# Performance work log

Hardware: AMD Instinct MI355X
Metric: run time of the kernel (lower is better)

Reference implementation:

```python
import jax, jax.numpy as jnp
import numpy as np

N, B, E, H = 16384, 16, 131072, 2
NPG = N // B  # nodes per graph
DIMS = [128, 256, 512]  # in==out channels per GAT layer


def setup_inputs() -> dict:
    key = jax.random.key(0)
    ks = iter(jax.random.split(key, 40))
    inp = {"node_feats": jax.random.normal(next(ks), (N, DIMS[0]), jnp.float32)}
    for l, d in enumerate(DIMS):
        s = 1.0 / np.sqrt(d)
        inp[f"W{l}"] = jax.random.normal(next(ks), (d, H * d), jnp.float32) * s
        inp[f"attnl{l}"] = jax.random.normal(next(ks), (H, d), jnp.float32) * 0.1
        inp[f"attnr{l}"] = jax.random.normal(next(ks), (H, d), jnp.float32) * 0.1
        inp[f"resW{l}"] = jax.random.normal(next(ks), (d, H * d), jnp.float32) * s
        inp[f"gamma{l}"] = jnp.ones((d,), jnp.float32)
        inp[f"beta{l}"] = jnp.zeros((d,), jnp.float32)
        inp[f"alpha{l}"] = jnp.ones((d,), jnp.float32)
    dst = jax.random.randint(next(ks), (E,), 0, N, jnp.int32)
    # source node sampled from the same graph as the destination
    src = (dst // NPG) * NPG + jax.random.randint(next(ks), (E,), 0, NPG, jnp.int32)
    inp["edge_src"] = src
    inp["edge_dst"] = dst
    inp["graph_ids"] = jnp.repeat(jnp.arange(B, dtype=jnp.int32), NPG)
    return inp


def _gat(x, W, al, ar, rW, src, dst, d):
    # x: [N, in]; W,rW: [in, H*d]; al,ar: [H,d]
    h = (x @ W).reshape(N, H, d)
    el = jnp.sum(h * al, -1)  # [N,H]
    er = jnp.sum(h * ar, -1)  # [N,H]
    e = jax.nn.leaky_relu(el[src] + er[dst], 0.2)  # [E,H]
    m = jax.ops.segment_max(e, dst, num_segments=N)
    ex = jnp.exp(e - m[dst])
    a = ex / jax.ops.segment_sum(ex, dst, num_segments=N)[dst]  # edge softmax
    out = jax.ops.segment_sum(h[src] * a[:, :, None], dst, num_segments=N)
    return out + (x @ rW).reshape(N, H, d)  # residual projection


def _gnorm(x, gamma, beta, alpha, eps=1e-5):
    # GraphNorm: (x - alpha*mean) / std * gamma + beta, stats over all nodes/heads
    mean = jnp.mean(x, axis=(0, 1), keepdims=True)
    sh = x - alpha * mean
    var = jnp.mean(sh * sh, axis=(0, 1), keepdims=True)
    return gamma * sh * jax.lax.rsqrt(var + eps) + beta


def reference(node_feats, W0, attnl0, attnr0, resW0, gamma0, beta0, alpha0,
              W1, attnl1, attnr1, resW1, gamma1, beta1, alpha1,
              W2, attnl2, attnr2, resW2, gamma2, beta2, alpha2,
              edge_src, edge_dst, graph_ids):
    params = [(W0, attnl0, attnr0, resW0, gamma0, beta0, alpha0),
              (W1, attnl1, attnr1, resW1, gamma1, beta1, alpha1),
              (W2, attnl2, attnr2, resW2, gamma2, beta2, alpha2)]
    counts = jax.ops.segment_sum(jnp.ones((N,), jnp.float32), graph_ids, num_segments=B)
    x = node_feats
    parts = []
    for l, d in enumerate(DIMS):
        W, al, ar, rW, g, b, a_ = params[l]
        x = _gat(x.reshape(N, -1), W, al, ar, rW, edge_src, edge_dst, d)  # [N,H,d]
        x = _gnorm(x, g, b, a_)
        x = jax.nn.leaky_relu(x, 0.01)
        nm = x.mean(1)  # [N,d] head-mean stored as 'updated_feats'
        parts.append(jax.ops.segment_sum(nm, graph_ids, num_segments=B) / counts[:, None])
    return jax.nn.leaky_relu(jnp.concatenate(parts, -1), 0.01)  # [B, 896]
```

## Files before the change

### kernel.cpp

```cpp
#include <hip/hip_runtime.h>
#include <math.h>

constexpr int NNODES  = 16384;
constexpr int NEDGES  = 131072;
constexpr int NGRAPHS = 16;

typedef short bf16x8 __attribute__((ext_vector_type(8)));
typedef short bf16x4 __attribute__((ext_vector_type(4)));
typedef float f32x4  __attribute__((ext_vector_type(4)));

__device__ __forceinline__ float leaky(float x, float s){ return x >= 0.0f ? x : s * x; }

__device__ __forceinline__ unsigned short f2bf(float f){
  unsigned u = __builtin_bit_cast(unsigned, f);
  u += 0x7FFFu + ((u >> 16) & 1u);
  return (unsigned short)(u >> 16);
}
__device__ __forceinline__ float bf2f(unsigned short u){
  unsigned x = (unsigned)u << 16; return __builtin_bit_cast(float, x);
}

__global__ void k_deg(const int* __restrict__ dst, int* __restrict__ deg){
  int e = blockIdx.x * 256 + threadIdx.x;
  if (e < NEDGES) atomicAdd(&deg[dst[e]], 1);
}

__global__ __launch_bounds__(1024) void k_scan(const int* __restrict__ deg,
                                               int* __restrict__ rowptr,
                                               int* __restrict__ cursor){
  __shared__ int sums[1024];
  int t = threadIdx.x;
  int loc[16];
  int s = 0;
  #pragma unroll
  for (int i = 0; i < 16; i++){ loc[i] = deg[t*16 + i]; s += loc[i]; }
  sums[t] = s; __syncthreads();
  for (int off = 1; off < 1024; off <<= 1){
    int v = (t >= off) ? sums[t - off] : 0;
    __syncthreads();
    sums[t] += v;
    __syncthreads();
  }
  int base = (t > 0) ? sums[t-1] : 0;
  #pragma unroll
  for (int i = 0; i < 16; i++){
    rowptr[t*16 + i] = base; cursor[t*16 + i] = base; base += loc[i];
  }
  if (t == 1023) rowptr[NNODES] = base;
}

__global__ void k_scatter(const int* __restrict__ src, const int* __restrict__ dst,
                          int* __restrict__ cursor, int* __restrict__ perm){
  int e = blockIdx.x * 256 + threadIdx.x;
  if (e < NEDGES){ int p = atomicAdd(&cursor[dst[e]], 1); perm[p] = src[e]; }
}

__global__ __launch_bounds__(256) void k_counts(const int* __restrict__ gid, float* __restrict__ counts){
  __shared__ int h[NGRAPHS];
  int t = threadIdx.x;
  if (t < NGRAPHS) h[t] = 0;
  __syncthreads();
  int base = blockIdx.x * 1024;
  #pragma unroll
  for (int i = 0; i < 4; i++)
    atomicAdd(&h[gid[base + t + i*256]], 1);
  __syncthreads();
  if (t < NGRAPHS && h[t] > 0) atomicAdd(&counts[t], (float)h[t]);
}

__global__ void k_cvt(const float* __restrict__ in, unsigned short* __restrict__ out, int n4){
  int i = blockIdx.x * 256 + threadIdx.x;
  if (i >= n4) return;
  float4 v = ((const float4*)in)[i];
  ushort4 o; o.x = f2bf(v.x); o.y = f2bf(v.y); o.z = f2bf(v.z); o.w = f2bf(v.w);
  ((ushort4*)out)[i] = o;
}

__global__ __launch_bounds__(256) void k_cvt_t(const float* __restrict__ W,
                                               unsigned short* __restrict__ Wt,
                                               int K, int NN){
  __shared__ float tile[32][33];
  int n0 = blockIdx.x * 32, k0 = blockIdx.y * 32;
  int tx = threadIdx.x & 31, ty = threadIdx.x >> 5;
  #pragma unroll
  for (int i = 0; i < 4; i++)
    tile[ty + i*8][tx] = W[(size_t)(k0 + ty + i*8) * NN + n0 + tx];
  __syncthreads();
  #pragma unroll
  for (int i = 0; i < 4; i++)
    Wt[(size_t)(n0 + ty + i*8) * K + k0 + tx] = f2bf(tile[tx][ty + i*8]);
}

template<bool BF16OUT>
__global__ __launch_bounds__(256) void k_gemm_bf16(const unsigned short* __restrict__ A,
                                                   const unsigned short* __restrict__ Bt,
                                                   void* __restrict__ Cv, int K, int NN){
  __shared__ unsigned short As[128 * 64];
  __shared__ unsigned short Bs[128 * 64];
  int t = threadIdx.x;
  int lane = t & 63, w = t >> 6;
  int wr = (w >> 1) * 64, wc = (w & 1) * 64;
  int l16 = lane & 15, lhi = lane >> 4;
  int rowA = blockIdx.y * 128;
  int colB = blockIdx.x * 128;
  f32x4 acc[4][4] = {};

  for (int k0 = 0; k0 < K; k0 += 64){
    __syncthreads();
    #pragma unroll
    for (int c = 0; c < 4; c++){
      int chunk = t + c * 256;
      int row = chunk >> 3, kc = (chunk & 7) * 8;
      int off = row * 128 + ((kc * 2) ^ ((row & 7) << 4));
      bf16x8 va = *(const bf16x8*)(A  + (size_t)(rowA + row) * K + k0 + kc);
      *(bf16x8*)((char*)As + off) = va;
      bf16x8 vb = *(const bf16x8*)(Bt + (size_t)(colB + row) * K + k0 + kc);
      *(bf16x8*)((char*)Bs + off) = vb;
    }
    __syncthreads();
    bf16x8 af[4][2], bfr[4][2];
    #pragma unroll
    for (int mi = 0; mi < 4; mi++){
      int row = wr + mi * 16 + l16;
      #pragma unroll
      for (int s = 0; s < 2; s++){
        int k = s * 32 + lhi * 8;
        int off = row * 128 + ((k * 2) ^ ((row & 7) << 4));
        af[mi][s] = *(const bf16x8*)((const char*)As + off);
      }
    }
    #pragma unroll
    for (int ni = 0; ni < 4; ni++){
      int row = wc + ni * 16 + l16;
      #pragma unroll
      for (int s = 0; s < 2; s++){
        int k = s * 32 + lhi * 8;
        int off = row * 128 + ((k * 2) ^ ((row & 7) << 4));
        bfr[ni][s] = *(const bf16x8*)((const char*)Bs + off);
      }
    }
    #pragma unroll
    for (int mi = 0; mi < 4; mi++)
      #pragma unroll
      for (int ni = 0; ni < 4; ni++){
        acc[mi][ni] = __builtin_amdgcn_mfma_f32_16x16x32_bf16(af[mi][0], bfr[ni][0], acc[mi][ni], 0, 0, 0);
        acc[mi][ni] = __builtin_amdgcn_mfma_f32_16x16x32_bf16(af[mi][1], bfr[ni][1], acc[mi][ni], 0, 0, 0);
      }
  }
  #pragma unroll
  for (int mi = 0; mi < 4; mi++){
    #pragma unroll
    for (int j = 0; j < 4; j++){
      int r = rowA + wr + mi * 16 + lhi * 4 + j;
      if (BF16OUT){
        unsigned short* Cp = (unsigned short*)Cv + (size_t)r * NN + colB + wc + l16;
        #pragma unroll
        for (int ni = 0; ni < 4; ni++)
          Cp[ni * 16] = f2bf(acc[mi][ni][j]);
      } else {
        float* Cp = (float*)Cv + (size_t)r * NN + colB + wc + l16;
        #pragma unroll
        for (int ni = 0; ni < 4; ni++)
          Cp[ni * 16] = acc[mi][ni][j];
      }
    }
  }
}

template<int D>
__global__ __launch_bounds__(256) void k_elr(const unsigned short* __restrict__ HB,
                                             const float* __restrict__ al,
                                             const float* __restrict__ ar,
                                             float* __restrict__ el, float* __restrict__ er){
  constexpr int ITER = (2*D)/256;
  int wid = threadIdx.x >> 6, lane = threadIdx.x & 63;
  int n = blockIdx.x * 4 + wid;
  const unsigned short* hrow = HB + (size_t)n * (2*D);
  float sl[2] = {0.f, 0.f}, sr[2] = {0.f, 0.f};
  #pragma unroll
  for (int j = 0; j < ITER; j++){
    int base = j*256 + lane*4;
    bf16x4 v = *(const bf16x4*)(hrow + base);
    int hh = (base < D) ? 0 : 1;
    #pragma unroll
    for (int i = 0; i < 4; i++){
      float f = bf2f((unsigned short)v[i]);
      sl[hh] += f * al[base + i];
      sr[hh] += f * ar[base + i];
    }
  }
  #pragma unroll
  for (int o = 32; o; o >>= 1){
    sl[0] += __shfl_xor(sl[0], o); sl[1] += __shfl_xor(sl[1], o);
    sr[0] += __shfl_xor(sr[0], o); sr[1] += __shfl_xor(sr[1], o);
  }
  if (lane < 2){ el[n*2 + lane] = sl[lane]; er[n*2 + lane] = sr[lane]; }
}

template<int D>
__global__ __launch_bounds__(256) void k_attn(const unsigned short* __restrict__ HB,
                                              float* __restrict__ RB,
                                              const float* __restrict__ el,
                                              const float* __restrict__ er,
                                              const int* __restrict__ rowptr,
                                              const int* __restrict__ perm){
  constexpr int ITER = (2*D)/256;
  int wid = threadIdx.x >> 6, lane = threadIdx.x & 63;
  int nb = (blockIdx.x & 7) * (NNODES/4/8) + (blockIdx.x >> 3);
  int n = nb * 4 + wid;
  int r0 = rowptr[n], r1 = rowptr[n+1];
  if (r0 == r1) return;
  float er0 = er[n*2], er1 = er[n*2+1];
  float mx0 = -1e30f, mx1 = -1e30f;
  for (int e = r0 + lane; e < r1; e += 64){
    int s = perm[e];
    mx0 = fmaxf(mx0, leaky(el[s*2]   + er0, 0.2f));
    mx1 = fmaxf(mx1, leaky(el[s*2+1] + er1, 0.2f));
  }
  #pragma unroll
  for (int o = 32; o; o >>= 1){ mx0 = fmaxf(mx0, __shfl_xor(mx0, o)); mx1 = fmaxf(mx1, __shfl_xor(mx1, o)); }
  float sm0 = 0.0f, sm1 = 0.0f;
  for (int e = r0 + lane; e < r1; e += 64){
    int s = perm[e];
    sm0 += expf(leaky(el[s*2]   + er0, 0.2f) - mx0);
    sm1 += expf(leaky(el[s*2+1] + er1, 0.2f) - mx1);
  }
  #pragma unroll
  for (int o = 32; o; o >>= 1){ sm0 += __shfl_xor(sm0, o); sm1 += __shfl_xor(sm1, o); }
  float inv0 = 1.0f / sm0, inv1 = 1.0f / sm1;
  float acc[ITER][4];
  #pragma unroll
  for (int j = 0; j < ITER; j++)
    #pragma unroll
    for (int i = 0; i < 4; i++) acc[j][i] = 0.0f;
  for (int e = r0; e < r1; ++e){
    int s = perm[e];
    float a0 = expf(leaky(el[s*2]   + er0, 0.2f) - mx0) * inv0;
    float a1 = expf(leaky(el[s*2+1] + er1, 0.2f) - mx1) * inv1;
    const unsigned short* hrow = HB + (size_t)s * (2*D);
    #pragma unroll
    for (int j = 0; j < ITER; j++){
      int base = j*256 + lane*4;
      bf16x4 v = *(const bf16x4*)(hrow + base);
      float a = (base < D) ? a0 : a1;
      #pragma unroll
      for (int i = 0; i < 4; i++)
        acc[j][i] += a * bf2f((unsigned short)v[i]);
    }
  }
  float* rrow = RB + (size_t)n * (2*D);
  #pragma unroll
  for (int j = 0; j < ITER; j++){
    int base = j*256 + lane*4;
    float4 r = *(float4*)(rrow + base);
    r.x += acc[j][0]; r.y += acc[j][1]; r.z += acc[j][2]; r.w += acc[j][3];
    *(float4*)(rrow + base) = r;
  }
}

__global__ __launch_bounds__(256) void k_stats(const float* __restrict__ R, int nn,
                                               float* __restrict__ gsum, float* __restrict__ gsq){
  int t = threadIdx.x, lane = t & 63, w = t >> 6;
  int c = blockIdx.y * 256 + lane * 4;
  const float* base = R + (size_t)(blockIdx.x * 128 + w) * nn + c;
  float4 s = make_float4(0,0,0,0), q = make_float4(0,0,0,0);
  #pragma unroll 4
  for (int i = 0; i < 32; i++){
    float4 v = *(const float4*)(base + (size_t)(i * 4) * nn);
    s.x += v.x; s.y += v.y; s.z += v.z; s.w += v.w;
    q.x += v.x*v.x; q.y += v.y*v.y; q.z += v.z*v.z; q.w += v.w*v.w;
  }
  __shared__ float4 rs[256], rq[256];
  rs[t] = s; rq[t] = q; __syncthreads();
  if (t < 64){
    float4 a = rs[t], b = rs[t+64], c2 = rs[t+128], d2 = rs[t+192];
    float4 e = rq[t], f = rq[t+64], g2 = rq[t+128], h2 = rq[t+192];
    int cc = blockIdx.y * 256 + t * 4;
    atomicAdd(&gsum[cc+0], a.x+b.x+c2.x+d2.x);
    atomicAdd(&gsum[cc+1], a.y+b.y+c2.y+d2.y);
    atomicAdd(&gsum[cc+2], a.z+b.z+c2.z+d2.z);
    atomicAdd(&gsum[cc+3], a.w+b.w+c2.w+d2.w);
    atomicAdd(&gsq [cc+0], e.x+f.x+g2.x+h2.x);
    atomicAdd(&gsq [cc+1], e.y+f.y+g2.y+h2.y);
    atomicAdd(&gsq [cc+2], e.z+f.z+g2.z+h2.z);
    atomicAdd(&gsq [cc+3], e.w+f.w+g2.w+h2.w);
  }
}

__global__ void k_finstats(const float* __restrict__ gsum, const float* __restrict__ gsq,
                           const float* __restrict__ alpha,
                           float* __restrict__ mean, float* __restrict__ rstd, int d){
  int t = threadIdx.x;
  if (t >= d) return;
  float s = gsum[t] + gsum[t + d];
  float q = gsq[t]  + gsq[t + d];
  const float M = (float)(2 * NNODES);
  float m   = s / M;
  float msq = q / M;
  float a   = alpha[t];
  float var = msq - a * m * m * (2.0f - a);
  mean[t] = m;
  rstd[t] = rsqrtf(var + 1e-5f);
}

__global__ __launch_bounds__(256) void k_norm_pool(const float* __restrict__ R,
                                                   unsigned short* __restrict__ Xn,
                                                   const float* __restrict__ mean,
                                                   const float* __restrict__ rstd,
                                                   const float* __restrict__ gamma,
                                                   const float* __restrict__ beta,
                                                   const float* __restrict__ alpha,
                                                   float* __restrict__ pool, int d, int loff){
  int t = threadIdx.x, lane = t & 63, w = t >> 6;
  int c = blockIdx.y * 256 + lane * 4;
  int cm = c & (d - 1);
  int nodeb = blockIdx.x * 128;
  int g = blockIdx.x >> 3;
  int nn = 2 * d;
  float4 mm = *(const float4*)(mean + cm);
  float4 rr = *(const float4*)(rstd + cm);
  float4 gg = *(const float4*)(gamma + cm);
  float4 bb = *(const float4*)(beta + cm);
  float4 aa = *(const float4*)(alpha + cm);
  float am0 = aa.x*mm.x, am1 = aa.y*mm.y, am2 = aa.z*mm.z, am3 = aa.w*mm.w;
  const float* base = R + (size_t)(nodeb + w) * nn + c;
  unsigned short* xb = Xn ? (Xn + (size_t)(nodeb + w) * nn + c) : nullptr;
  float4 accp = make_float4(0,0,0,0);
  #pragma unroll 4
  for (int i = 0; i < 32; i++){
    float4 v = *(const float4*)(base + (size_t)(i * 4) * nn);
    float y0 = gg.x*(v.x-am0)*rr.x + bb.x; y0 = y0 >= 0.f ? y0 : 0.01f*y0;
    float y1 = gg.y*(v.y-am1)*rr.y + bb.y; y1 = y1 >= 0.f ? y1 : 0.01f*y1;
    float y2 = gg.z*(v.z-am2)*rr.z + bb.z; y2 = y2 >= 0.f ? y2 : 0.01f*y2;
    float y3 = gg.w*(v.w-am3)*rr.w + bb.w; y3 = y3 >= 0.f ? y3 : 0.01f*y3;
    if (xb){
      ushort4 o; o.x = f2bf(y0); o.y = f2bf(y1); o.z = f2bf(y2); o.w = f2bf(y3);
      *(ushort4*)(xb + (size_t)(i * 4) * nn) = o;
    }
    accp.x += y0; accp.y += y1; accp.z += y2; accp.w += y3;
  }
  __shared__ float4 red[256];
  red[t] = accp; __syncthreads();
  if (t < 64){
    float4 a = red[t], b = red[t+64], c2 = red[t+128], d2 = red[t+192];
    int cc = blockIdx.y * 256 + t * 4;
    float* pb = pool + g * 896 + loff;
    atomicAdd(&pb[(cc+0) & (d-1)], 0.5f*(a.x+b.x+c2.x+d2.x));
    atomicAdd(&pb[(cc+1) & (d-1)], 0.5f*(a.y+b.y+c2.y+d2.y));
    atomicAdd(&pb[(cc+2) & (d-1)], 0.5f*(a.z+b.z+c2.z+d2.z));
    atomicAdd(&pb[(cc+3) & (d-1)], 0.5f*(a.w+b.w+c2.w+d2.w));
  }
}

__global__ void k_final(const float* __restrict__ pool, const float* __restrict__ counts,
                        float* __restrict__ out){
  int idx = blockIdx.x * 256 + threadIdx.x;
  if (idx >= NGRAPHS * 896) return;
  int g = idx / 896;
  float v = pool[idx] / counts[g];
  out[idx] = v >= 0.0f ? v : 0.01f * v;
}

extern "C" void kernel_launch(void* const* d_in, const int* in_sizes, int n_in,
                              void* d_out, int out_size, void* d_ws, size_t ws_size,
                              hipStream_t stream){
  const float* x0 = (const float*)d_in[0];
  const float *W[3], *AL[3], *AR[3], *RW[3], *GA[3], *BE[3], *ALP[3];
  for (int l = 0; l < 3; l++){
    const int b = 1 + l*7;
    W[l]  = (const float*)d_in[b+0];
    AL[l] = (const float*)d_in[b+1];
    AR[l] = (const float*)d_in[b+2];
    RW[l] = (const float*)d_in[b+3];
    GA[l] = (const float*)d_in[b+4];
    BE[l] = (const float*)d_in[b+5];
    ALP[l]= (const float*)d_in[b+6];
  }
  const int* esrc = (const int*)d_in[22];
  const int* edst = (const int*)d_in[23];
  const int* gid  = (const int*)d_in[24];
  float* out = (float*)d_out;

  char* p = (char*)d_ws;
  auto carve = [&](size_t bytes)->void*{
    void* r = (void*)p; p += (bytes + 255) & ~(size_t)255; return r;
  };
  unsigned short* HB = (unsigned short*)carve((size_t)NNODES * 1024 * 2);
  float* RB     = (float*)carve((size_t)NNODES * 1024 * 4);
  unsigned short* X0b = (unsigned short*)carve((size_t)NNODES * 128 * 2);
  unsigned short* XA  = (unsigned short*)carve((size_t)NNODES * 256 * 2);
  unsigned short* XB  = (unsigned short*)carve((size_t)NNODES * 512 * 2);
  unsigned short* Wt  = (unsigned short*)carve((size_t)1024 * 512 * 2);
  unsigned short* RWt = (unsigned short*)carve((size_t)1024 * 512 * 2);
  float* el     = (float*)carve((size_t)NNODES * 2 * 4);
  float* er     = (float*)carve((size_t)NNODES * 2 * 4);
  int*   deg    = (int*)  carve((size_t)NNODES * 4);
  int*   rowptr = (int*)  carve((size_t)(NNODES + 1) * 4);
  int*   cursor = (int*)  carve((size_t)NNODES * 4);
  int*   perm   = (int*)  carve((size_t)NEDGES * 4);
  float* stats  = (float*)carve(2048 * 4);
  float* meanb  = (float*)carve(512 * 4);
  float* rstdb  = (float*)carve(512 * 4);
  float* pool   = (float*)carve((size_t)NGRAPHS * 896 * 4);
  float* countsF= (float*)carve((size_t)NGRAPHS * 4);
  (void)ws_size; (void)in_sizes; (void)n_in; (void)out_size;

  hipMemsetAsync(deg, 0, NNODES * 4, stream);
  hipMemsetAsync(pool, 0, NGRAPHS * 896 * 4, stream);
  hipMemsetAsync(countsF, 0, NGRAPHS * 4, stream);

  k_deg    <<<NEDGES/256, 256, 0, stream>>>(edst, deg);
  k_scan   <<<1, 1024, 0, stream>>>(deg, rowptr, cursor);
  k_scatter<<<NEDGES/256, 256, 0, stream>>>(esrc, edst, cursor, perm);
  k_counts <<<NNODES/1024, 256, 0, stream>>>(gid, countsF);
  k_cvt    <<<(NNODES*128/4 + 255)/256, 256, 0, stream>>>(x0, X0b, NNODES*128/4);

  const unsigned short* xin = X0b;
  int loff = 0;
  const int dims[3] = {128, 256, 512};
  for (int l = 0; l < 3; l++){
    int d = dims[l], nn = 2*d;
    dim3 gt(nn/32, d/32);
    k_cvt_t<<<gt, 256, 0, stream>>>(W[l],  Wt,  d, nn);
    k_cvt_t<<<gt, 256, 0, stream>>>(RW[l], RWt, d, nn);
    dim3 gg(nn/128, NNODES/128);
    k_gemm_bf16<true> <<<gg, 256, 0, stream>>>(xin, Wt,  HB, d, nn);
    k_gemm_bf16<false><<<gg, 256, 0, stream>>>(xin, RWt, RB, d, nn);
    if (d == 128){
      k_elr <128><<<NNODES/4, 256, 0, stream>>>(HB, AL[l], AR[l], el, er);
      k_attn<128><<<NNODES/4, 256, 0, stream>>>(HB, RB, el, er, rowptr, perm);
    } else if (d == 256){
      k_elr <256><<<NNODES/4, 256, 0, stream>>>(HB, AL[l], AR[l], el, er);
      k_attn<256><<<NNODES/4, 256, 0, stream>>>(HB, RB, el, er, rowptr, perm);
    } else {
      k_elr <512><<<NNODES/4, 256, 0, stream>>>(HB, AL[l], AR[l], el, er);
      k_attn<512><<<NNODES/4, 256, 0, stream>>>(HB, RB, el, er, rowptr, perm);
    }
    hipMemsetAsync(stats, 0, 2048 * 4, stream);
    dim3 gs(NNODES/128, nn/256);
    k_stats   <<<gs, 256, 0, stream>>>(RB, nn, stats, stats + 1024);
    k_finstats<<<1, 512, 0, stream>>>(stats, stats + 1024, ALP[l], meanb, rstdb, d);
    unsigned short* xn = (l == 0) ? XA : (l == 1) ? XB : nullptr;
    k_norm_pool<<<gs, 256, 0, stream>>>(RB, xn, meanb, rstdb, GA[l], BE[l], ALP[l], pool, d, loff);
    xin = xn; loff += d;
  }
  k_final<<<(NGRAPHS*896 + 255)/256, 256, 0, stream>>>(pool, countsF, out);
}
```

Before: 387.7 us.

## Merge W and residual GEMMs into one launch with direct global-to-LDS loads

The two per-layer GEMMs (x@W into bf16 HB and x@resW into fp32 RB) become one kernel whose grid spans both weight matrices. Each block picks its weight and output by column index. Tile staging now uses global_load_lds, writing 16-byte chunks straight into swizzled LDS instead of going through registers. Block IDs are remapped in groups of 8, which changes the order tiles are scheduled across the GPU and may improve L2 reuse of the A rows. The intent is to cut launch count, register pressure and load latency in the staging path, at the risk of getting the LDS address and swizzle mapping of the direct loads wrong.

```diff
diff --git a/kernel.cpp b/kernel.cpp
--- a/kernel.cpp
+++ b/kernel.cpp
@@ -18,6 +18,11 @@
 }
 __device__ __forceinline__ float bf2f(unsigned short u){
   unsigned x = (unsigned)u << 16; return __builtin_bit_cast(float, x);
+}
+
+__device__ __forceinline__ void gload_lds16(const unsigned short* g, unsigned short* l){
+  __builtin_amdgcn_global_load_lds((const __attribute__((address_space(1))) void*)g,
+                                   (__attribute__((address_space(3))) void*)l, 16, 0, 0);
 }
 
 __global__ void k_deg(const int* __restrict__ dst, int* __restrict__ deg){
@@ -91,31 +96,41 @@
     Wt[(size_t)(n0 + ty + i*8) * K + k0 + tx] = f2bf(tile[tx][ty + i*8]);
 }
 
-template<bool BF16OUT>
-__global__ __launch_bounds__(256) void k_gemm_bf16(const unsigned short* __restrict__ A,
-                                                   const unsigned short* __restrict__ Bt,
-                                                   void* __restrict__ Cv, int K, int NN){
+__global__ __launch_bounds__(256) void k_gemm2(const unsigned short* __restrict__ A,
+                                               const unsigned short* __restrict__ Wt,
+                                               const unsigned short* __restrict__ RWt,
+                                               unsigned short* __restrict__ HB,
+                                               float* __restrict__ RB,
+                                               int K, int NN){
   __shared__ unsigned short As[128 * 64];
   __shared__ unsigned short Bs[128 * 64];
   int t = threadIdx.x;
   int lane = t & 63, w = t >> 6;
+  int nx  = gridDim.x;
+  int nwg = nx * gridDim.y;
+  int bid = blockIdx.x + blockIdx.y * nx;
+  int wg  = (bid & 7) * (nwg >> 3) + (bid >> 3);
+  int bx = wg % nx, by = wg / nx;
+  int half = nx >> 1;
+  bool isW = bx < half;
+  const unsigned short* Bt = isW ? Wt : RWt;
+  int colB = (isW ? bx : bx - half) * 128;
+  int rowA = by * 128;
+
   int wr = (w >> 1) * 64, wc = (w & 1) * 64;
   int l16 = lane & 15, lhi = lane >> 4;
-  int rowA = blockIdx.y * 128;
-  int colB = blockIdx.x * 128;
+  int r8  = lane >> 3;
+  int kcs = (((lane & 7) * 16) ^ (r8 << 4)) >> 1;
   f32x4 acc[4][4] = {};
 
   for (int k0 = 0; k0 < K; k0 += 64){
     __syncthreads();
     #pragma unroll
-    for (int c = 0; c < 4; c++){
-      int chunk = t + c * 256;
-      int row = chunk >> 3, kc = (chunk & 7) * 8;
-      int off = row * 128 + ((kc * 2) ^ ((row & 7) << 4));
-      bf16x8 va = *(const bf16x8*)(A  + (size_t)(rowA + row) * K + k0 + kc);
-      *(bf16x8*)((char*)As + off) = va;
-      bf16x8 vb = *(const bf16x8*)(Bt + (size_t)(colB + row) * K + k0 + kc);
-      *(bf16x8*)((char*)Bs + off) = vb;
+    for (int i = 0; i < 4; i++){
+      int c = w * 4 + i;
+      int row = c * 8 + r8;
+      gload_lds16(A  + (size_t)(rowA + row) * K + k0 + kcs, &As[c * 512]);
+      gload_lds16(Bt + (size_t)(colB + row) * K + k0 + kcs, &Bs[c * 512]);
     }
     __syncthreads();
     bf16x8 af[4][2], bfr[4][2];
@@ -152,13 +167,13 @@
     #pragma unroll
     for (int j = 0; j < 4; j++){
       int r = rowA + wr + mi * 16 + lhi * 4 + j;
-      if (BF16OUT){
-        unsigned short* Cp = (unsigned short*)Cv + (size_t)r * NN + colB + wc + l16;
+      if (isW){
+        unsigned short* Cp = HB + (size_t)r * NN + colB + wc + l16;
         #pragma unroll
         for (int ni = 0; ni < 4; ni++)
           Cp[ni * 16] = f2bf(acc[mi][ni][j]);
       } else {
-        float* Cp = (float*)Cv + (size_t)r * NN + colB + wc + l16;
+        float* Cp = RB + (size_t)r * NN + colB + wc + l16;
         #pragma unroll
         for (int ni = 0; ni < 4; ni++)
           Cp[ni * 16] = acc[mi][ni][j];
@@ -423,9 +438,8 @@
     dim3 gt(nn/32, d/32);
     k_cvt_t<<<gt, 256, 0, stream>>>(W[l],  Wt,  d, nn);
     k_cvt_t<<<gt, 256, 0, stream>>>(RW[l], RWt, d, nn);
-    dim3 gg(nn/128, NNODES/128);
-    k_gemm_bf16<true> <<<gg, 256, 0, stream>>>(xin, Wt,  HB, d, nn);
-    k_gemm_bf16<false><<<gg, 256, 0, stream>>>(xin, RWt, RB, d, nn);
+    dim3 gg(2*nn/128, NNODES/128);
+    k_gemm2<<<gg, 256, 0, stream>>>(xin, Wt, RWt, HB, RB, d, nn);
     if (d == 128){
       k_elr <128><<<NNODES/4, 256, 0, stream>>>(HB, AL[l], AR[l], el, er);
       k_attn<128><<<NNODES/4, 256, 0, stream>>>(HB, RB, el, er, rowptr, perm);
```

New measurement: 367.9 us. 5.1% less time.
